# Performance work log

Hardware: AMD Instinct MI355X
Metric: run time of the kernel (lower is better)

The kernel has to match this reference:

```python
import jax, jax.numpy as jnp
import numpy as np

B, N, D, K = 8, 4096, 128, 1024


def setup_inputs() -> dict:
    key = jax.random.key(0)
    kx, kp = jax.random.split(key)
    x = jax.random.normal(kx, (B, N, D), dtype=jnp.float32)
    # matches nn.Parameter(...).uniform_(-0.1, 0.1)
    prototypes = jax.random.uniform(kp, (K, D), dtype=jnp.float32, minval=-0.1, maxval=0.1)
    return {"x": x, "prototypes": prototypes, "hard": 1}


def reference(x, prototypes, hard):
    x_sq = jnp.sum(x * x, axis=-1, keepdims=True)            # [B,N,1]
    p_sq = jnp.sum(prototypes * prototypes, axis=-1)         # [K]
    xp = jnp.einsum('bnd,kd->bnk', x, prototypes)            # [B,N,K]
    scores = -(x_sq + p_sq[None, None, :] - 2.0 * xp)        # [B,N,K]
    if bool(hard):
        idx = jnp.argmax(scores, axis=-1)                    # [B,N]
        matched = prototypes[idx]                            # [B,N,D]
    else:
        w = jax.nn.softmax(scores, axis=-1)                  # [B,N,K]
        matched = jnp.einsum('bnk,kd->bnd', w, prototypes)   # [B,N,D]
    return (matched, scores)
```

## Files before the change

### kernel.cpp

```cpp
#include <hip/hip_runtime.h>

typedef short short8 __attribute__((ext_vector_type(8)));
typedef float f32x4  __attribute__((ext_vector_type(4)));

constexpr int M_TOT  = 8 * 4096;
constexpr int K_PROT = 1024;
constexpr int D_DIM  = 128;

constexpr size_t WS_PSQ_OFF = (size_t)M_TOT * 4;
constexpr size_t WS_PF_OFF  = WS_PSQ_OFF + (size_t)K_PROT * 4;

constexpr int NORM_BLOCKS  = (M_TOT + K_PROT) / 8;
constexpr int PFRAG_BLOCKS = 16384 / 256;

__device__ inline unsigned short bf16_rne(float f) {
  unsigned u = __builtin_bit_cast(unsigned, f);
  unsigned r = u + 0x7FFFu + ((u >> 16) & 1u);
  return (unsigned short)(r >> 16);
}

__device__ inline void barrier_lds() {
  asm volatile("s_waitcnt lgkmcnt(0)\n\ts_barrier" ::: "memory");
}

__global__ __launch_bounds__(256) void prep_kernel(
    const float* __restrict__ x, const float* __restrict__ p,
    float* __restrict__ xsq, float* __restrict__ psq, short* __restrict__ pf) {
  const int bx  = blockIdx.x;
  const int tid = threadIdx.x;
  if (bx < NORM_BLOCKS) {
    int group = bx * 8 + (tid >> 5);
    int lane  = tid & 31;
    if (group >= M_TOT + K_PROT) return;
    const float* row = (group < M_TOT) ? (x + (size_t)group * D_DIM)
                                       : (p + (size_t)(group - M_TOT) * D_DIM);
    float4 v = reinterpret_cast<const float4*>(row)[lane];
    float s = v.x * v.x + v.y * v.y + v.z * v.z + v.w * v.w;
    #pragma unroll
    for (int off = 16; off > 0; off >>= 1) s += __shfl_down(s, off, 32);
    if (lane == 0) {
      if (group < M_TOT) xsq[group] = s;
      else psq[group - M_TOT] = s;
    }
  } else {
    int g    = (bx - NORM_BLOCKS) * 256 + tid;
    int lane = g & 63;
    int ks   = (g >> 6) & 3;
    int ng   = g >> 8;
    int proto = ng * 16 + (lane & 15);
    int k0    = ks * 32 + (lane >> 4) * 8;
    const float4* pr = (const float4*)(p + (size_t)proto * D_DIM + k0);
    float4 a = pr[0], b = pr[1];
    float e[8] = {a.x, a.y, a.z, a.w, b.x, b.y, b.z, b.w};
    short8 frag;
    #pragma unroll
    for (int j = 0; j < 8; ++j) frag[j] = (short)bf16_rne(e[j]);
    *(short8*)(pf + (size_t)g * 8) = frag;
  }
}

__global__ __launch_bounds__(256, 2) void proto_mfma(
    const float* __restrict__ x, const float* __restrict__ p,
    const short* __restrict__ pf, const float* __restrict__ xsq,
    const float* __restrict__ psq,
    float* __restrict__ matched, float* __restrict__ scores) {
  __shared__ short xlds[16 * 64 * 8];
  __shared__ float sbuf[64][132];
  __shared__ float sv[4][64];
  __shared__ int   si[4][64];
  __shared__ int   fidx[64];

  const int tid  = threadIdx.x;
  const int w    = tid >> 6;
  const int l    = tid & 63;
  const int m0   = blockIdx.x * 64;
  const int csub = (l >> 4) << 2;

  #pragma unroll
  for (int i = 0; i < 4; ++i) {
    int piece = i * 256 + tid;
    int s = piece >> 6;
    int ks = s & 3, nt = s >> 2;
    int pix = m0 + nt * 16 + (l & 15);
    int k0  = ks * 32 + (l >> 4) * 8;
    const float4* xr = (const float4*)(x + (size_t)pix * D_DIM + k0);
    float4 a = xr[0], b = xr[1];
    float e[8] = {a.x, a.y, a.z, a.w, b.x, b.y, b.z, b.w};
    short8 frag;
    #pragma unroll
    for (int j = 0; j < 8; ++j) frag[j] = (short)bf16_rne(e[j]);
    *(short8*)(xlds + (size_t)piece * 8) = frag;
  }
  __syncthreads();

  float xs[4];
  #pragma unroll
  for (int nt = 0; nt < 4; ++nt) xs[nt] = xsq[m0 + nt * 16 + (l & 15)];

  float best[4]; int bidx[4];
  #pragma unroll
  for (int nt = 0; nt < 4; ++nt) { best[nt] = -3.4e38f; bidx[nt] = 0; }

  for (int chunk = 0; chunk < 4; ++chunk) {
    f32x4 acc[4][4];
    #pragma unroll
    for (int mt = 0; mt < 4; ++mt)
      #pragma unroll
      for (int nt = 0; nt < 4; ++nt) acc[mt][nt] = (f32x4){0.f, 0.f, 0.f, 0.f};

    const int pgbase = chunk * 16 + w * 4;

    #pragma unroll
    for (int ks = 0; ks < 4; ++ks) {
      short8 pah[4], bh[4];
      #pragma unroll
      for (int mt = 0; mt < 4; ++mt)
        pah[mt] = *(const short8*)(pf + ((size_t)((pgbase + mt) * 4 + ks) * 64 + l) * 8);
      #pragma unroll
      for (int nt = 0; nt < 4; ++nt)
        bh[nt] = *(const short8*)(xlds + (size_t)(((nt * 4 + ks) * 64) + l) * 8);
      #pragma unroll
      for (int mt = 0; mt < 4; ++mt)
        #pragma unroll
        for (int nt = 0; nt < 4; ++nt)
          acc[mt][nt] = __builtin_amdgcn_mfma_f32_16x16x32_bf16(pah[mt], bh[nt], acc[mt][nt], 0, 0, 0);
    }

    #pragma unroll
    for (int mt = 0; mt < 4; ++mt) {
      int pbase = chunk * 256 + w * 64 + mt * 16 + csub;
      float psa[4];
      *(float4*)psa = *(const float4*)(psq + pbase);
      #pragma unroll
      for (int nt = 0; nt < 4; ++nt) {
        f32x4 o;
        {
          #pragma clang fp contract(off)
          #pragma unroll
          for (int r = 0; r < 4; ++r) {
            float t = (xs[nt] + psa[r]) - 2.0f * acc[mt][nt][r];
            o[r] = -t;
            if (o[r] > best[nt]) { best[nt] = o[r]; bidx[nt] = pbase + r; }
          }
        }
        acc[mt][nt] = o;
      }
    }

    #pragma unroll
    for (int h = 0; h < 2; ++h) {
      if ((w >> 1) == h) {
        const int colbase = (w & 1) * 64 + csub;
        #pragma unroll
        for (int mt = 0; mt < 4; ++mt)
          #pragma unroll
          for (int nt = 0; nt < 4; ++nt)
            *(f32x4*)&sbuf[nt * 16 + (l & 15)][colbase + mt * 16] = acc[mt][nt];
      }
      barrier_lds();
      const int gbase = chunk * 256 + h * 128;
      #pragma unroll
      for (int ps = 0; ps < 8; ++ps) {
        int idx = ps * 256 + tid;
        int row = idx >> 5;
        int f4  = idx & 31;
        f32x4 v = *(const f32x4*)&sbuf[row][f4 * 4];
        *((f32x4*)(scores + (size_t)(m0 + row) * K_PROT + gbase + f4 * 4)) = v;
      }
      barrier_lds();
    }
  }

  #pragma unroll
  for (int nt = 0; nt < 4; ++nt) {
    #pragma unroll
    for (int m = 16; m <= 32; m <<= 1) {
      float ov = __shfl_xor(best[nt], m);
      int   oi = __shfl_xor(bidx[nt], m);
      if (ov > best[nt] || (ov == best[nt] && oi < bidx[nt])) {
        best[nt] = ov; bidx[nt] = oi;
      }
    }
  }
  if (l < 16) {
    #pragma unroll
    for (int nt = 0; nt < 4; ++nt) {
      sv[w][nt * 16 + l] = best[nt];
      si[w][nt * 16 + l] = bidx[nt];
    }
  }
  __syncthreads();
  if (tid < 64) {
    float v = sv[0][tid]; int bi = si[0][tid];
    #pragma unroll
    for (int e = 1; e < 4; ++e) {
      float vv = sv[e][tid]; int ii = si[e][tid];
      if (vv > v || (vv == v && ii < bi)) { v = vv; bi = ii; }
    }
    fidx[tid] = bi;
  }
  __syncthreads();

  for (int q = tid; q < 64 * 32; q += 256) {
    int pix = q >> 5, f4 = q & 31;
    float4 v = ((const float4*)(p + (size_t)fidx[pix] * D_DIM))[f4];
    *((f32x4*)(matched + (size_t)(m0 + pix) * D_DIM) + f4) = *(f32x4*)&v;
  }
}

extern "C" void kernel_launch(void* const* d_in, const int* in_sizes, int n_in,
                              void* d_out, int out_size, void* d_ws, size_t ws_size,
                              hipStream_t stream) {
  const float* x = (const float*)d_in[0];
  const float* p = (const float*)d_in[1];

  float* matched = (float*)d_out;
  float* scores  = (float*)d_out + (size_t)M_TOT * D_DIM;

  float* xsq = (float*)d_ws;
  float* psq = (float*)((char*)d_ws + WS_PSQ_OFF);
  short* pf  = (short*)((char*)d_ws + WS_PF_OFF);

  prep_kernel<<<NORM_BLOCKS + PFRAG_BLOCKS, 256, 0, stream>>>(x, p, xsq, psq, pf);
  proto_mfma<<<M_TOT / 64, 256, 0, stream>>>(x, p, pf, xsq, psq, matched, scores);
}
```

Before: 171.0 us.

## Fuse x norm computation into main kernel and double block to 8 waves

Removes the separate x squared-norm pass from the prep kernel and computes per-row partial sums while x is loaded and converted to bf16 in the main kernel, reducing them through reused LDS. The main kernel now runs 512 threads with each wave owning two prototype tiles instead of four, lowering accumulator register pressure and raising wave count. This avoids an extra full read of x and a workspace round-trip, at the cost of an extra block barrier and more per-block LDS reduction work.

New measurement: 167.4 us. 1.02x faster.

```diff
diff --git a/kernel.cpp b/kernel.cpp
--- a/kernel.cpp
+++ b/kernel.cpp
@@ -7,10 +7,9 @@
 constexpr int K_PROT = 1024;
 constexpr int D_DIM  = 128;
 
-constexpr size_t WS_PSQ_OFF = (size_t)M_TOT * 4;
-constexpr size_t WS_PF_OFF  = WS_PSQ_OFF + (size_t)K_PROT * 4;
-
-constexpr int NORM_BLOCKS  = (M_TOT + K_PROT) / 8;
+constexpr size_t WS_PF_OFF = (size_t)K_PROT * 4;
+
+constexpr int PSQ_BLOCKS   = K_PROT / 8;
 constexpr int PFRAG_BLOCKS = 16384 / 256;
 
 __device__ inline unsigned short bf16_rne(float f) {
@@ -24,26 +23,21 @@
 }
 
 __global__ __launch_bounds__(256) void prep_kernel(
-    const float* __restrict__ x, const float* __restrict__ p,
-    float* __restrict__ xsq, float* __restrict__ psq, short* __restrict__ pf) {
+    const float* __restrict__ p, float* __restrict__ psq,
+    short* __restrict__ pf) {
   const int bx  = blockIdx.x;
   const int tid = threadIdx.x;
-  if (bx < NORM_BLOCKS) {
+  if (bx < PSQ_BLOCKS) {
     int group = bx * 8 + (tid >> 5);
     int lane  = tid & 31;
-    if (group >= M_TOT + K_PROT) return;
-    const float* row = (group < M_TOT) ? (x + (size_t)group * D_DIM)
-                                       : (p + (size_t)(group - M_TOT) * D_DIM);
-    float4 v = reinterpret_cast<const float4*>(row)[lane];
+    if (group >= K_PROT) return;
+    float4 v = reinterpret_cast<const float4*>(p + (size_t)group * D_DIM)[lane];
     float s = v.x * v.x + v.y * v.y + v.z * v.z + v.w * v.w;
     #pragma unroll
     for (int off = 16; off > 0; off >>= 1) s += __shfl_down(s, off, 32);
-    if (lane == 0) {
-      if (group < M_TOT) xsq[group] = s;
-      else psq[group - M_TOT] = s;
-    }
+    if (lane == 0) psq[group] = s;
   } else {
-    int g    = (bx - NORM_BLOCKS) * 256 + tid;
+    int g    = (bx - PSQ_BLOCKS) * 256 + tid;
     int lane = g & 63;
     int ks   = (g >> 6) & 3;
     int ng   = g >> 8;
@@ -59,16 +53,16 @@
   }
 }
 
-__global__ __launch_bounds__(256, 2) void proto_mfma(
+__global__ __launch_bounds__(512, 4) void proto_mfma(
     const float* __restrict__ x, const float* __restrict__ p,
-    const short* __restrict__ pf, const float* __restrict__ xsq,
-    const float* __restrict__ psq,
+    const short* __restrict__ pf, const float* __restrict__ psq,
     float* __restrict__ matched, float* __restrict__ scores) {
   __shared__ short xlds[16 * 64 * 8];
   __shared__ float sbuf[64][132];
-  __shared__ float sv[4][64];
-  __shared__ int   si[4][64];
+  __shared__ float sv[8][64];
+  __shared__ int   si[8][64];
   __shared__ int   fidx[64];
+  __shared__ float xsqv[64];
 
   const int tid  = threadIdx.x;
   const int w    = tid >> 6;
@@ -76,9 +70,11 @@
   const int m0   = blockIdx.x * 64;
   const int csub = (l >> 4) << 2;
 
-  #pragma unroll
-  for (int i = 0; i < 4; ++i) {
-    int piece = i * 256 + tid;
+  float (*xpart)[16] = (float(*)[16])&sbuf[0][0];
+
+  #pragma unroll
+  for (int i = 0; i < 2; ++i) {
+    int piece = i * 512 + tid;
     int s = piece >> 6;
     int ks = s & 3, nt = s >> 2;
     int pix = m0 + nt * 16 + (l & 15);
@@ -86,6 +82,9 @@
     const float4* xr = (const float4*)(x + (size_t)pix * D_DIM + k0);
     float4 a = xr[0], b = xr[1];
     float e[8] = {a.x, a.y, a.z, a.w, b.x, b.y, b.z, b.w};
+    float ss = e[0]*e[0] + e[1]*e[1] + e[2]*e[2] + e[3]*e[3]
+             + e[4]*e[4] + e[5]*e[5] + e[6]*e[6] + e[7]*e[7];
+    xpart[nt * 16 + (l & 15)][ks * 4 + (l >> 4)] = ss;
     short8 frag;
     #pragma unroll
     for (int j = 0; j < 8; ++j) frag[j] = (short)bf16_rne(e[j]);
@@ -93,42 +92,50 @@
   }
   __syncthreads();
 
+  if (tid < 64) {
+    float s = 0.f;
+    #pragma unroll
+    for (int j = 0; j < 16; ++j) s += xpart[tid][j];
+    xsqv[tid] = s;
+  }
+  __syncthreads();
+
   float xs[4];
   #pragma unroll
-  for (int nt = 0; nt < 4; ++nt) xs[nt] = xsq[m0 + nt * 16 + (l & 15)];
+  for (int nt = 0; nt < 4; ++nt) xs[nt] = xsqv[nt * 16 + (l & 15)];
 
   float best[4]; int bidx[4];
   #pragma unroll
   for (int nt = 0; nt < 4; ++nt) { best[nt] = -3.4e38f; bidx[nt] = 0; }
 
   for (int chunk = 0; chunk < 4; ++chunk) {
-    f32x4 acc[4][4];
-    #pragma unroll
-    for (int mt = 0; mt < 4; ++mt)
+    f32x4 acc[2][4];
+    #pragma unroll
+    for (int mt = 0; mt < 2; ++mt)
       #pragma unroll
       for (int nt = 0; nt < 4; ++nt) acc[mt][nt] = (f32x4){0.f, 0.f, 0.f, 0.f};
 
-    const int pgbase = chunk * 16 + w * 4;
+    const int pgbase = chunk * 16 + w * 2;
 
     #pragma unroll
     for (int ks = 0; ks < 4; ++ks) {
-      short8 pah[4], bh[4];
-      #pragma unroll
-      for (int mt = 0; mt < 4; ++mt)
+      short8 pah[2], bh[4];
+      #pragma unroll
+      for (int mt = 0; mt < 2; ++mt)
         pah[mt] = *(const short8*)(pf + ((size_t)((pgbase + mt) * 4 + ks) * 64 + l) * 8);
       #pragma unroll
       for (int nt = 0; nt < 4; ++nt)
         bh[nt] = *(const short8*)(xlds + (size_t)(((nt * 4 + ks) * 64) + l) * 8);
       #pragma unroll
-      for (int mt = 0; mt < 4; ++mt)
+      for (int mt = 0; mt < 2; ++mt)
         #pragma unroll
         for (int nt = 0; nt < 4; ++nt)
           acc[mt][nt] = __builtin_amdgcn_mfma_f32_16x16x32_bf16(pah[mt], bh[nt], acc[mt][nt], 0, 0, 0);
     }
 
     #pragma unroll
-    for (int mt = 0; mt < 4; ++mt) {
-      int pbase = chunk * 256 + w * 64 + mt * 16 + csub;
+    for (int mt = 0; mt < 2; ++mt) {
+      int pbase = chunk * 256 + w * 32 + mt * 16 + csub;
       float psa[4];
       *(float4*)psa = *(const float4*)(psq + pbase);
       #pragma unroll
@@ -149,10 +156,10 @@
 
     #pragma unroll
     for (int h = 0; h < 2; ++h) {
-      if ((w >> 1) == h) {
-        const int colbase = (w & 1) * 64 + csub;
+      if ((w >> 2) == h) {
+        const int colbase = (w & 3) * 32 + csub;
         #pragma unroll
-        for (int mt = 0; mt < 4; ++mt)
+        for (int mt = 0; mt < 2; ++mt)
           #pragma unroll
           for (int nt = 0; nt < 4; ++nt)
             *(f32x4*)&sbuf[nt * 16 + (l & 15)][colbase + mt * 16] = acc[mt][nt];
@@ -160,8 +167,8 @@
       barrier_lds();
       const int gbase = chunk * 256 + h * 128;
       #pragma unroll
-      for (int ps = 0; ps < 8; ++ps) {
-        int idx = ps * 256 + tid;
+      for (int ps = 0; ps < 4; ++ps) {
+        int idx = ps * 512 + tid;
         int row = idx >> 5;
         int f4  = idx & 31;
         f32x4 v = *(const f32x4*)&sbuf[row][f4 * 4];
@@ -193,7 +200,7 @@
   if (tid < 64) {
     float v = sv[0][tid]; int bi = si[0][tid];
     #pragma unroll
-    for (int e = 1; e < 4; ++e) {
+    for (int e = 1; e < 8; ++e) {
       float vv = sv[e][tid]; int ii = si[e][tid];
       if (vv > v || (vv == v && ii < bi)) { v = vv; bi = ii; }
     }
@@ -201,7 +208,9 @@
   }
   __syncthreads();
 
-  for (int q = tid; q < 64 * 32; q += 256) {
+  #pragma unroll
+  for (int q0 = 0; q0 < 4; ++q0) {
+    int q = q0 * 512 + tid;
     int pix = q >> 5, f4 = q & 31;
     float4 v = ((const float4*)(p + (size_t)fidx[pix] * D_DIM))[f4];
     *((f32x4*)(matched + (size_t)(m0 + pix) * D_DIM) + f4) = *(f32x4*)&v;
@@ -217,10 +226,9 @@
   float* matched = (float*)d_out;
   float* scores  = (float*)d_out + (size_t)M_TOT * D_DIM;
 
-  float* xsq = (float*)d_ws;
-  float* psq = (float*)((char*)d_ws + WS_PSQ_OFF);
+  float* psq = (float*)d_ws;
   short* pf  = (short*)((char*)d_ws + WS_PF_OFF);
 
-  prep_kernel<<<NORM_BLOCKS + PFRAG_BLOCKS, 256, 0, stream>>>(x, p, xsq, psq, pf);
-  proto_mfma<<<M_TOT / 64, 256, 0, stream>>>(x, p, pf, xsq, psq, matched, scores);
-}
+  prep_kernel<<<PSQ_BLOCKS + PFRAG_BLOCKS, 256, 0, stream>>>(p, psq, pf);
+  proto_mfma<<<M_TOT / 64, 512, 0, stream>>>(x, p, pf, psq, matched, scores);
+}
```
